# Kernel tuning notes

Hardware: AMD Instinct MI355X
Metric: run time of the kernel (lower is better)

The kernel has to match this reference:

```python
import jax, jax.numpy as jnp
import numpy as np

DIM = 768
HEADS = 12

def setup_inputs() -> dict:
    key = jax.random.key(0)
    ks = jax.random.split(key, 5)
    x = jax.random.normal(ks[0], (8, 1024, DIM), dtype=jnp.float32)
    s = 1.0 / np.sqrt(DIM)
    W_qkv = jax.random.normal(ks[1], (DIM, 3 * DIM), dtype=jnp.float32) * s
    b_qkv = jax.random.normal(ks[2], (3 * DIM,), dtype=jnp.float32) * 0.01
    W_proj = jax.random.normal(ks[3], (DIM, DIM), dtype=jnp.float32) * s
    b_proj = jax.random.normal(ks[4], (DIM,), dtype=jnp.float32) * 0.01
    return {"x": x, "W_qkv": W_qkv, "b_qkv": b_qkv, "W_proj": W_proj, "b_proj": b_proj}

def reference(x, W_qkv, b_qkv, W_proj, b_proj):
    B, T, D = x.shape
    H = HEADS
    hd = D // H
    scale = hd ** -0.5
    qkv = x @ W_qkv + b_qkv                      # [B,T,3D]
    qkv = qkv.reshape(B, T, 3, H, hd)
    q, k, v = jnp.moveaxis(qkv, 2, 0)            # each [B,T,H,hd]
    q = jnp.transpose(q, (0, 2, 1, 3))           # [B,H,T,hd]
    k = jnp.transpose(k, (0, 2, 1, 3))
    v = jnp.transpose(v, (0, 2, 1, 3))
    attn = jnp.einsum('bhqd,bhkd->bhqk', q, k) * scale
    attn = jax.nn.softmax(attn, axis=-1)
    y = jnp.einsum('bhqk,bhkd->bhqd', attn, v)   # [B,H,T,hd]
    y = jnp.transpose(y, (0, 2, 1, 3)).reshape(B, T, D)
    return y @ W_proj + b_proj
```

## Files before the change

### kernel.cpp

```cpp
#include <hip/hip_runtime.h>

typedef unsigned short u16;
typedef __attribute__((ext_vector_type(8))) short short8;
typedef __attribute__((ext_vector_type(4))) short short4v;
typedef __attribute__((ext_vector_type(2))) int int2v;
typedef __attribute__((ext_vector_type(4))) float f32x4;

#define DIM   768
#define HEADS 12
#define HD    64
#define BATCH 8
#define SEQ   1024
#define MTOK  (BATCH*SEQ)
#define NQKV  (3*DIM)
#define KPAD  72
#define EPAD  66
#define PSZ   ((size_t)BATCH*HEADS*SEQ*HD)
#define SCQ   0.1803368801f

__device__ __forceinline__ u16 f2bf(float f) {
  unsigned x = __float_as_uint(f);
  x += 0x7fffu + ((x >> 16) & 1u);
  return (u16)(x >> 16);
}

__device__ __forceinline__ void gload16(const u16* g, u16* l) {
  __builtin_amdgcn_global_load_lds(
      (const __attribute__((address_space(1))) unsigned int*)g,
      (__attribute__((address_space(3))) unsigned int*)l, 16, 0, 0);
}

#define XBLK 6144
#define QTBLK 1728
__global__ void cvt_all_k(const float* __restrict__ x,
                          const float* __restrict__ Wqkv,
                          const float* __restrict__ Wproj,
                          u16* __restrict__ xb, u16* __restrict__ wqkvt,
                          u16* __restrict__ wprojt) {
  __shared__ u16 tile[32][33];
  const int blk = blockIdx.x;
  if (blk < XBLK) {
    const int i = blk * 256 + threadIdx.x;
    float4 f = ((const float4*)x)[i];
    short4v o;
    o.x = (short)f2bf(f.x); o.y = (short)f2bf(f.y);
    o.z = (short)f2bf(f.z); o.w = (short)f2bf(f.w);
    ((short4v*)xb)[i] = o;
    return;
  }
  const float* in; u16* out; int K, N, n0, k0;
  if (blk < XBLK + QTBLK) {
    const int t = blk - XBLK;
    in = Wqkv; out = wqkvt; K = DIM; N = NQKV;
    n0 = (t % (NQKV / 32)) * 32; k0 = (t / (NQKV / 32)) * 32;
  } else {
    const int t = blk - XBLK - QTBLK;
    in = Wproj; out = wprojt; K = DIM; N = DIM;
    n0 = (t % (DIM / 32)) * 32; k0 = (t / (DIM / 32)) * 32;
  }
  const int tx = threadIdx.x & 31, ty = threadIdx.x >> 5;
  #pragma unroll
  for (int i = 0; i < 32; i += 8)
    tile[ty + i][tx] = f2bf(in[(size_t)(k0 + ty + i) * N + n0 + tx]);
  __syncthreads();
  #pragma unroll
  for (int i = 0; i < 32; i += 8)
    out[(size_t)(n0 + ty + i) * K + k0 + tx] = tile[tx][ty + i];
}

__global__ __launch_bounds__(256, 2)
void gemm_qkv(const u16* __restrict__ A, const u16* __restrict__ Bt,
              const float* __restrict__ bias, u16* __restrict__ qkv) {
  __shared__ __align__(16) u16 smem[2 * 256 * 32 + 2 * 128 * 32];
  u16* lA0 = smem;
  u16* lA1 = smem + 256 * 32;
  u16* lB0 = smem + 2 * 256 * 32;
  u16* lB1 = lB0 + 128 * 32;
  const int w = threadIdx.x >> 6, lane = threadIdx.x & 63;
  const int l15 = lane & 15, quad = lane >> 4;
  const int m0 = blockIdx.y * 256, n0 = blockIdx.x * 128;
  const int wm = (w >> 1) * 128, wn = (w & 1) * 64;

  f32x4 acc[8][4] = {};

  const int ar = threadIdx.x >> 2, ak = (threadIdx.x & 3) * 8;
  const u16* ga = A  + (size_t)(m0 + ar) * DIM + ak;
  const u16* gb = Bt + (size_t)(n0 + ar) * DIM + ak;
  const int lo = threadIdx.x * 8;

  for (int k0 = 0; k0 < DIM; k0 += 64) {
    #pragma unroll
    for (int t = 0; t < 4; ++t) {
      gload16(ga + (size_t)t * 64 * DIM + k0,      lA0 + lo + t * 2048);
      gload16(ga + (size_t)t * 64 * DIM + k0 + 32, lA1 + lo + t * 2048);
    }
    #pragma unroll
    for (int t = 0; t < 2; ++t) {
      gload16(gb + (size_t)t * 64 * DIM + k0,      lB0 + lo + t * 2048);
      gload16(gb + (size_t)t * 64 * DIM + k0 + 32, lB1 + lo + t * 2048);
    }
    __syncthreads();

    #pragma unroll
    for (int kh = 0; kh < 2; ++kh) {
      const u16* lAh = kh ? lA1 : lA0;
      const u16* lBh = kh ? lB1 : lB0;
      short8 af[8], bfr[4];
      #pragma unroll
      for (int mt = 0; mt < 8; ++mt)
        af[mt] = *(const short8*)&lAh[(wm + mt * 16 + l15) * 32 + quad * 8];
      #pragma unroll
      for (int nt = 0; nt < 4; ++nt)
        bfr[nt] = *(const short8*)&lBh[(wn + nt * 16 + l15) * 32 + quad * 8];
      #pragma unroll
      for (int mt = 0; mt < 8; ++mt)
        #pragma unroll
        for (int nt = 0; nt < 4; ++nt)
          acc[mt][nt] = __builtin_amdgcn_mfma_f32_16x16x32_bf16(af[mt], bfr[nt], acc[mt][nt], 0, 0, 0);
    }
    __syncthreads();
  }

  const int bb = m0 >> 10;
  const int tb0 = (m0 & 1023) + wm;
  const int nh = n0 + wn;
  const int part = nh / DIM, idx = nh - part * DIM;
  const int h = idx >> 6;
  u16* dstbase = qkv + part * PSZ + ((size_t)(bb * HEADS + h) * SEQ + tb0) * HD;
  const float qsc = (part == 0) ? SCQ : 1.0f;

  float bnl[4];
  #pragma unroll
  for (int nt = 0; nt < 4; ++nt) bnl[nt] = bias[nh + nt * 16 + l15];

  const int erow = lane >> 3, ec8 = (lane & 7) * 8;
  #pragma unroll
  for (int mt = 0; mt < 8; ++mt) {
    u16* ep = smem + w * (16 * EPAD) + (mt & 1) * (4 * 16 * EPAD);
    #pragma unroll
    for (int nt = 0; nt < 4; ++nt)
      #pragma unroll
      for (int r = 0; r < 4; ++r)
        ep[(quad * 4 + r) * EPAD + nt * 16 + l15] = f2bf((acc[mt][nt][r] + bnl[nt]) * qsc);
    #pragma unroll
    for (int j = 0; j < 2; ++j) {
      const int trow = j * 8 + erow;
      short8 vrow = *(const short8*)&ep[trow * EPAD + ec8];
      *(short8*)(dstbase + (size_t)(mt * 16 + trow) * HD + ec8) = vrow;
    }
  }
}

__global__ void vt_k(const u16* __restrict__ v, u16* __restrict__ vt) {
  __shared__ u16 tl[64][72];
  const int bh = blockIdx.y, t0 = blockIdx.x * 64;
  #pragma unroll
  for (int i = 0; i < 2; ++i) {
    const int c = threadIdx.x + i * 256;
    const int tr = c >> 3, dc8 = c & 7;
    const int cc = dc8 ^ (tr >> 3);
    *(short8*)&tl[tr][cc * 8] = *(const short8*)(v + ((size_t)bh * SEQ + t0 + tr) * HD + dc8 * 8);
  }
  __syncthreads();
  #pragma unroll
  for (int i = 0; i < 2; ++i) {
    const int c = threadIdx.x + i * 256;
    const int dr = c >> 3, tc = (c & 7) * 8;
    short8 outv;
    #pragma unroll
    for (int j = 0; j < 8; ++j) {
      const int t = tc + j;
      const int cc = (dr >> 3) ^ (t >> 3);
      outv[j] = (short)tl[t][cc * 8 + (dr & 7)];
    }
    *(short8*)(vt + ((size_t)bh * HD + dr) * SEQ + t0 + tc) = outv;
  }
}

__global__ __launch_bounds__(256)
void gemm_proj(const u16* __restrict__ A, const u16* __restrict__ Bt,
               const float* __restrict__ bias, float* __restrict__ outF) {
  __shared__ __align__(16) u16 smem[4 * 128 * 32];
  u16* lA0 = smem;
  u16* lA1 = smem + 128 * 32;
  u16* lB0 = smem + 2 * 128 * 32;
  u16* lB1 = smem + 3 * 128 * 32;
  const int w = threadIdx.x >> 6, lane = threadIdx.x & 63;
  const int l15 = lane & 15, quad = lane >> 4;
  const int m0 = blockIdx.y * 128, n0 = blockIdx.x * 128;
  const int wm = (w >> 1) * 64, wn = (w & 1) * 64;

  f32x4 acc[4][4] = {};

  const int ar = threadIdx.x >> 2, ak = (threadIdx.x & 3) * 8;
  const u16* ga = A  + (size_t)(m0 + ar) * DIM + ak;
  const u16* gb = Bt + (size_t)(n0 + ar) * DIM + ak;
  const int lo = threadIdx.x * 8;

  for (int k0 = 0; k0 < DIM; k0 += 64) {
    #pragma unroll
    for (int t = 0; t < 2; ++t) {
      gload16(ga + (size_t)t * 64 * DIM + k0,      lA0 + lo + t * 2048);
      gload16(ga + (size_t)t * 64 * DIM + k0 + 32, lA1 + lo + t * 2048);
      gload16(gb + (size_t)t * 64 * DIM + k0,      lB0 + lo + t * 2048);
      gload16(gb + (size_t)t * 64 * DIM + k0 + 32, lB1 + lo + t * 2048);
    }
    __syncthreads();

    #pragma unroll
    for (int kh = 0; kh < 2; ++kh) {
      const u16* lAh = kh ? lA1 : lA0;
      const u16* lBh = kh ? lB1 : lB0;
      short8 af[4], bfr[4];
      #pragma unroll
      for (int mt = 0; mt < 4; ++mt)
        af[mt] = *(const short8*)&lAh[(wm + mt * 16 + l15) * 32 + quad * 8];
      #pragma unroll
      for (int nt = 0; nt < 4; ++nt)
        bfr[nt] = *(const short8*)&lBh[(wn + nt * 16 + l15) * 32 + quad * 8];
      #pragma unroll
      for (int mt = 0; mt < 4; ++mt)
        #pragma unroll
        for (int nt = 0; nt < 4; ++nt)
          acc[mt][nt] = __builtin_amdgcn_mfma_f32_16x16x32_bf16(af[mt], bfr[nt], acc[mt][nt], 0, 0, 0);
    }
    __syncthreads();
  }

  #pragma unroll
  for (int nt = 0; nt < 4; ++nt) {
    const int n = n0 + wn + nt * 16 + l15;
    const float bn = bias[n];
    #pragma unroll
    for (int mt = 0; mt < 4; ++mt)
      #pragma unroll
      for (int r = 0; r < 4; ++r) {
        const int m = m0 + wm + mt * 16 + quad * 4 + r;
        outF[(size_t)m * DIM + n] = acc[mt][nt][r] + bn;
      }
  }
}

__global__ __launch_bounds__(256)
void attn_k(const u16* __restrict__ qb, const u16* __restrict__ kb,
            const u16* __restrict__ vtb, u16* __restrict__ yb) {
  const int qt = blockIdx.x, bh = blockIdx.y;
  const int w = threadIdx.x >> 6, lane = threadIdx.x & 63;
  const int l15 = lane & 15, quad = lane >> 4;

  __shared__ __align__(16) u16 lK[64 * KPAD];
  __shared__ __align__(16) u16 lV[64 * KPAD];
  __shared__ __align__(16) u16 lP[4][32 * KPAD];

  const u16* qb0 = qb + ((size_t)bh * SEQ + qt * 128 + w * 32 + l15) * HD;
  short8 aq[2][2];
  #pragma unroll
  for (int qg = 0; qg < 2; ++qg) {
    aq[qg][0] = *(const short8*)(qb0 + (size_t)qg * 16 * HD + quad * 8);
    aq[qg][1] = *(const short8*)(qb0 + (size_t)qg * 16 * HD + 32 + quad * 8);
  }

  f32x4 o[2][4] = {};
  float rs[2] = {0.f, 0.f};

  const u16* kcbase = kb + (size_t)bh * SEQ * HD;
  const u16* vbase  = vtb + (size_t)bh * HD * SEQ;
  u16* lPw = &lP[w][0];

  for (int kc = 0; kc < 16; ++kc) {
    const u16* kg = kcbase + kc * 64 * HD;
    #pragma unroll
    for (int i = 0; i < 2; ++i) {
      const int cid = threadIdx.x + i * 256;
      *(short8*)&lK[(cid >> 3) * KPAD + (cid & 7) * 8] = *(const short8*)(kg + cid * 8);
    }
    #pragma unroll
    for (int i = 0; i < 2; ++i) {
      const int cid = threadIdx.x + i * 256;
      const int d = cid >> 3, c8 = (cid & 7) * 8;
      *(short8*)&lV[d * KPAD + c8] = *(const short8*)(vbase + (size_t)d * SEQ + kc * 64 + c8);
    }
    __syncthreads();

    short8 ak0[4], ak1[4], bv0[4], bv1[4];
    #pragma unroll
    for (int nt = 0; nt < 4; ++nt) {
      ak0[nt] = *(const short8*)&lK[(nt * 16 + l15) * KPAD + quad * 8];
      ak1[nt] = *(const short8*)&lK[(nt * 16 + l15) * KPAD + 32 + quad * 8];
      bv0[nt] = *(const short8*)&lV[(nt * 16 + l15) * KPAD + quad * 8];
      bv1[nt] = *(const short8*)&lV[(nt * 16 + l15) * KPAD + 32 + quad * 8];
    }

    #pragma unroll
    for (int qg = 0; qg < 2; ++qg) {
      f32x4 st[4] = {};
      #pragma unroll
      for (int nt = 0; nt < 4; ++nt) {
        st[nt] = __builtin_amdgcn_mfma_f32_16x16x32_bf16(ak0[nt], aq[qg][0], st[nt], 0, 0, 0);
        st[nt] = __builtin_amdgcn_mfma_f32_16x16x32_bf16(ak1[nt], aq[qg][1], st[nt], 0, 0, 0);
      }

      #pragma unroll
      for (int nt = 0; nt < 4; ++nt) {
        float p0 = __builtin_amdgcn_exp2f(st[nt][0]);
        float p1 = __builtin_amdgcn_exp2f(st[nt][1]);
        float p2 = __builtin_amdgcn_exp2f(st[nt][2]);
        float p3 = __builtin_amdgcn_exp2f(st[nt][3]);
        float t0 = __uint_as_float(__float_as_uint(p0) & 0xffff0000u);
        float t1 = __uint_as_float(__float_as_uint(p1) & 0xffff0000u);
        float t2 = __uint_as_float(__float_as_uint(p2) & 0xffff0000u);
        float t3 = __uint_as_float(__float_as_uint(p3) & 0xffff0000u);
        rs[qg] += (t0 + t1) + (t2 + t3);
        int2v pk;
        pk.x = (int)__builtin_amdgcn_perm(__float_as_uint(p1), __float_as_uint(p0), 0x07060302u);
        pk.y = (int)__builtin_amdgcn_perm(__float_as_uint(p3), __float_as_uint(p2), 0x07060302u);
        *(int2v*)&lPw[(qg * 16 + l15) * KPAD + nt * 16 + quad * 4] = pk;
      }
      const short8 ap0 = *(const short8*)&lPw[(qg * 16 + l15) * KPAD + quad * 8];
      const short8 ap1 = *(const short8*)&lPw[(qg * 16 + l15) * KPAD + 32 + quad * 8];
      #pragma unroll
      for (int nt = 0; nt < 4; ++nt) {
        o[qg][nt] = __builtin_amdgcn_mfma_f32_16x16x32_bf16(ap0, bv0[nt], o[qg][nt], 0, 0, 0);
        o[qg][nt] = __builtin_amdgcn_mfma_f32_16x16x32_bf16(ap1, bv1[nt], o[qg][nt], 0, 0, 0);
      }
    }
    __syncthreads();
  }

  const int b = bh / HEADS, h = bh % HEADS;
  #pragma unroll
  for (int qg = 0; qg < 2; ++qg) {
    rs[qg] += __shfl_xor(rs[qg], 16);
    rs[qg] += __shfl_xor(rs[qg], 32);
    #pragma unroll
    for (int r = 0; r < 4; ++r) {
      const float inv = 1.0f / __shfl(rs[qg], quad * 4 + r, 16);
      #pragma unroll
      for (int nt = 0; nt < 4; ++nt)
        lPw[(qg * 16 + quad * 4 + r) * KPAD + nt * 16 + l15] = f2bf(o[qg][nt][r] * inv);
    }
  }

  u16* dst = yb + ((size_t)b * SEQ + qt * 128 + w * 32) * DIM + h * HD;
  const int erow = lane >> 3, ec8 = (lane & 7) * 8;
  #pragma unroll
  for (int j = 0; j < 4; ++j) {
    const int trow = j * 8 + erow;
    short8 vrow = *(const short8*)&lPw[trow * KPAD + ec8];
    *(short8*)(dst + (size_t)trow * DIM + ec8) = vrow;
  }
}

extern "C" void kernel_launch(void* const* d_in, const int* in_sizes, int n_in,
                              void* d_out, int out_size, void* d_ws, size_t ws_size,
                              hipStream_t stream) {
  const float* x     = (const float*)d_in[0];
  const float* Wqkv  = (const float*)d_in[1];
  const float* bqkv  = (const float*)d_in[2];
  const float* Wproj = (const float*)d_in[3];
  const float* bproj = (const float*)d_in[4];
  float* out = (float*)d_out;

  u16* xb     = (u16*)d_ws;
  u16* wqkvt  = xb + (size_t)MTOK * DIM;
  u16* wprojt = wqkvt + (size_t)NQKV * DIM;
  u16* qkv_b  = wprojt + (size_t)DIM * DIM;
  u16* y_b    = qkv_b + 3 * PSZ;
  u16* vt_b   = xb;

  cvt_all_k<<<XBLK + QTBLK + (DIM / 32) * (DIM / 32), 256, 0, stream>>>(
      x, Wqkv, Wproj, xb, wqkvt, wprojt);

  gemm_qkv<<<dim3(NQKV / 128, MTOK / 256), 256, 0, stream>>>(xb, wqkvt, bqkv, qkv_b);

  vt_k<<<dim3(SEQ / 64, BATCH * HEADS), 256, 0, stream>>>(qkv_b + 2 * PSZ, vt_b);

  attn_k<<<dim3(SEQ / 128, BATCH * HEADS), 256, 0, stream>>>(
      qkv_b, qkv_b + PSZ, vt_b, y_b);

  gemm_proj<<<dim3(DIM / 128, MTOK / 128), 256, 0, stream>>>(y_b, wprojt, bproj, out);
}
```

Baseline: 202.8 us.

## Shrink QKV GEMM tile to 128x128 and register-prefetch K/V in attention

```diff
diff --git a/kernel.cpp b/kernel.cpp
--- a/kernel.cpp
+++ b/kernel.cpp
@@ -68,20 +68,20 @@
     out[(size_t)(n0 + ty + i) * K + k0 + tx] = tile[tx][ty + i];
 }
 
-__global__ __launch_bounds__(256, 2)
+__global__ __launch_bounds__(256)
 void gemm_qkv(const u16* __restrict__ A, const u16* __restrict__ Bt,
               const float* __restrict__ bias, u16* __restrict__ qkv) {
-  __shared__ __align__(16) u16 smem[2 * 256 * 32 + 2 * 128 * 32];
+  __shared__ __align__(16) u16 smem[4 * 128 * 32];
   u16* lA0 = smem;
-  u16* lA1 = smem + 256 * 32;
-  u16* lB0 = smem + 2 * 256 * 32;
-  u16* lB1 = lB0 + 128 * 32;
+  u16* lA1 = smem + 128 * 32;
+  u16* lB0 = smem + 2 * 128 * 32;
+  u16* lB1 = smem + 3 * 128 * 32;
   const int w = threadIdx.x >> 6, lane = threadIdx.x & 63;
   const int l15 = lane & 15, quad = lane >> 4;
-  const int m0 = blockIdx.y * 256, n0 = blockIdx.x * 128;
-  const int wm = (w >> 1) * 128, wn = (w & 1) * 64;
-
-  f32x4 acc[8][4] = {};
+  const int m0 = blockIdx.y * 128, n0 = blockIdx.x * 128;
+  const int wm = (w >> 1) * 64, wn = (w & 1) * 64;
+
+  f32x4 acc[4][4] = {};
 
   const int ar = threadIdx.x >> 2, ak = (threadIdx.x & 3) * 8;
   const u16* ga = A  + (size_t)(m0 + ar) * DIM + ak;
@@ -90,12 +90,9 @@
 
   for (int k0 = 0; k0 < DIM; k0 += 64) {
     #pragma unroll
-    for (int t = 0; t < 4; ++t) {
+    for (int t = 0; t < 2; ++t) {
       gload16(ga + (size_t)t * 64 * DIM + k0,      lA0 + lo + t * 2048);
       gload16(ga + (size_t)t * 64 * DIM + k0 + 32, lA1 + lo + t * 2048);
-    }
-    #pragma unroll
-    for (int t = 0; t < 2; ++t) {
       gload16(gb + (size_t)t * 64 * DIM + k0,      lB0 + lo + t * 2048);
       gload16(gb + (size_t)t * 64 * DIM + k0 + 32, lB1 + lo + t * 2048);
     }
@@ -105,15 +102,15 @@
     for (int kh = 0; kh < 2; ++kh) {
       const u16* lAh = kh ? lA1 : lA0;
       const u16* lBh = kh ? lB1 : lB0;
-      short8 af[8], bfr[4];
-      #pragma unroll
-      for (int mt = 0; mt < 8; ++mt)
+      short8 af[4], bfr[4];
+      #pragma unroll
+      for (int mt = 0; mt < 4; ++mt)
         af[mt] = *(const short8*)&lAh[(wm + mt * 16 + l15) * 32 + quad * 8];
       #pragma unroll
       for (int nt = 0; nt < 4; ++nt)
         bfr[nt] = *(const short8*)&lBh[(wn + nt * 16 + l15) * 32 + quad * 8];
       #pragma unroll
-      for (int mt = 0; mt < 8; ++mt)
+      for (int mt = 0; mt < 4; ++mt)
         #pragma unroll
         for (int nt = 0; nt < 4; ++nt)
           acc[mt][nt] = __builtin_amdgcn_mfma_f32_16x16x32_bf16(af[mt], bfr[nt], acc[mt][nt], 0, 0, 0);
@@ -135,7 +132,7 @@
 
   const int erow = lane >> 3, ec8 = (lane & 7) * 8;
   #pragma unroll
-  for (int mt = 0; mt < 8; ++mt) {
+  for (int mt = 0; mt < 4; ++mt) {
     u16* ep = smem + w * (16 * EPAD) + (mt & 1) * (4 * 16 * EPAD);
     #pragma unroll
     for (int nt = 0; nt < 4; ++nt)
@@ -267,20 +264,29 @@
   const u16* vbase  = vtb + (size_t)bh * HD * SEQ;
   u16* lPw = &lP[w][0];
 
+  const int cid0 = threadIdx.x, cid1 = threadIdx.x + 256;
+  const int sofs0 = (cid0 >> 3) * KPAD + (cid0 & 7) * 8;
+  const int sofs1 = (cid1 >> 3) * KPAD + (cid1 & 7) * 8;
+  const u16* vg0 = vbase + (size_t)(cid0 >> 3) * SEQ + (cid0 & 7) * 8;
+  const u16* vg1 = vbase + (size_t)(cid1 >> 3) * SEQ + (cid1 & 7) * 8;
+
+  short8 pk0 = *(const short8*)(kcbase + cid0 * 8);
+  short8 pk1 = *(const short8*)(kcbase + cid1 * 8);
+  short8 pv0 = *(const short8*)vg0;
+  short8 pv1 = *(const short8*)vg1;
+
   for (int kc = 0; kc < 16; ++kc) {
-    const u16* kg = kcbase + kc * 64 * HD;
-    #pragma unroll
-    for (int i = 0; i < 2; ++i) {
-      const int cid = threadIdx.x + i * 256;
-      *(short8*)&lK[(cid >> 3) * KPAD + (cid & 7) * 8] = *(const short8*)(kg + cid * 8);
-    }
-    #pragma unroll
-    for (int i = 0; i < 2; ++i) {
-      const int cid = threadIdx.x + i * 256;
-      const int d = cid >> 3, c8 = (cid & 7) * 8;
-      *(short8*)&lV[d * KPAD + c8] = *(const short8*)(vbase + (size_t)d * SEQ + kc * 64 + c8);
-    }
-    __syncthreads();
+    *(short8*)&lK[sofs0] = pk0;
+    *(short8*)&lK[sofs1] = pk1;
+    *(short8*)&lV[sofs0] = pv0;
+    *(short8*)&lV[sofs1] = pv1;
+    __syncthreads();
+
+    const int kn = (kc < 15) ? kc + 1 : 15;
+    pk0 = *(const short8*)(kcbase + kn * 64 * HD + cid0 * 8);
+    pk1 = *(const short8*)(kcbase + kn * 64 * HD + cid1 * 8);
+    pv0 = *(const short8*)(vg0 + kn * 64);
+    pv1 = *(const short8*)(vg1 + kn * 64);
 
     short8 ak0[4], ak1[4], bv0[4], bv1[4];
     #pragma unroll
@@ -371,7 +377,7 @@
   cvt_all_k<<<XBLK + QTBLK + (DIM / 32) * (DIM / 32), 256, 0, stream>>>(
       x, Wqkv, Wproj, xb, wqkvt, wprojt);
 
-  gemm_qkv<<<dim3(NQKV / 128, MTOK / 256), 256, 0, stream>>>(xb, wqkvt, bqkv, qkv_b);
+  gemm_qkv<<<dim3(NQKV / 128, MTOK / 128), 256, 0, stream>>>(xb, wqkvt, bqkv, qkv_b);
 
   vt_k<<<dim3(SEQ / 64, BATCH * HEADS), 256, 0, stream>>>(qkv_b + 2 * PSZ, vt_b);
 
```

After: 206.3 us. About the same (+1.7%).
